# Optimization experiments

Hardware: AMD Instinct MI355X
Metric: run time of the kernel (lower is better)

The kernel has to match this reference:

```python
import jax, jax.numpy as jnp
import numpy as np

B, SQ, SK = 2, 2048, 2048
D = 1024            # in_features == num_heads * head_size
H, HS = 16, 64      # num_heads, head_size
SCALE = HS ** -0.5


def setup_inputs() -> dict:
    key = jax.random.key(0)
    ks = jax.random.split(key, 10)
    s = 0.02
    return {
        "inputs": jax.random.normal(ks[0], (B, SQ, D), jnp.float32),
        "context": jax.random.normal(ks[1], (B, SK, D), jnp.float32),
        "Wq": jax.random.normal(ks[2], (D, D), jnp.float32) * s,
        "bq": jnp.zeros((D,), jnp.float32),
        "Wk": jax.random.normal(ks[3], (D, D), jnp.float32) * s,
        "bk": jnp.zeros((D,), jnp.float32),
        "Wv": jax.random.normal(ks[4], (D, D), jnp.float32) * s,
        "bv": jnp.zeros((D,), jnp.float32),
        "Wo": jax.random.normal(ks[5], (D, D), jnp.float32) * s,
        "bo": jnp.zeros((D,), jnp.float32),
    }


def reference(inputs, context, Wq, bq, Wk, bk, Wv, bv, Wo, bo):
    # QKV projections (torch Linear: x @ W.T + b; here W stored as [in, out])
    q = inputs @ Wq + bq            # [B, SQ, D]
    k = context @ Wk + bk           # [B, SK, D]
    v = context @ Wv + bv           # [B, SK, D]
    q = q.reshape(B, SQ, H, HS)
    k = k.reshape(B, SK, H, HS)
    v = v.reshape(B, SK, H, HS)
    # scores: [B, H, SQ, SK] -- full score matrix materialized (as in source)
    score = jnp.einsum("bqhd,bkhd->bhqk", q, k) * SCALE
    weights = jax.nn.softmax(score, axis=-1)
    attn = jnp.einsum("bhqk,bkhd->bqhd", weights, v)  # [B, SQ, H, HS]
    out = attn.reshape(B, SQ, H * HS)
    return out @ Wo + bo
```

## Files before the change

kernel.cpp:

```cpp
#include <hip/hip_runtime.h>

#define BB 2
#define SQ 2048
#define SK 2048
#define DD 1024
#define HH 16
#define HS 64
#define SCALE 0.125f
#define LOG2E 1.4426950408889634f

typedef __bf16 bf16x8 __attribute__((ext_vector_type(8)));
typedef float f32x4 __attribute__((ext_vector_type(4)));
typedef unsigned int uint;

#if defined(__has_builtin)
#if __has_builtin(__builtin_amdgcn_exp2f)
#define FEXP2(x) __builtin_amdgcn_exp2f(x)
#endif
#endif
#ifndef FEXP2
extern "C" __device__ float __ocml_native_exp2_f32(float);
#define FEXP2(x) __ocml_native_exp2_f32(x)
#endif

__device__ __forceinline__ void gload_lds16(const __bf16* g, __bf16* l) {
    __builtin_amdgcn_global_load_lds((const __attribute__((address_space(1))) uint*)(g),
                                     (__attribute__((address_space(3))) uint*)(l), 16, 0, 0);
}

__global__ void cast2_f32_bf16(const float* __restrict__ in0, const float* __restrict__ in1,
                               __bf16* __restrict__ out0, __bf16* __restrict__ out1, int n8each) {
    int i = blockIdx.x * blockDim.x + threadIdx.x;
    const float* src;
    __bf16* dst;
    int j;
    if (i < n8each) { src = in0; dst = out0; j = i; }
    else            { src = in1; dst = out1; j = i - n8each; }
    const float4* p = ((const float4*)src) + (size_t)j * 2;
    float4 a = p[0], b = p[1];
    bf16x8 v = {(__bf16)a.x, (__bf16)a.y, (__bf16)a.z, (__bf16)a.w,
                (__bf16)b.x, (__bf16)b.y, (__bf16)b.z, (__bf16)b.w};
    ((bf16x8*)dst)[j] = v;
}

__global__ void wtrans(const float* __restrict__ W0, const float* __restrict__ W1,
                       const float* __restrict__ W2, const float* __restrict__ W3,
                       __bf16* __restrict__ Wt) {
    __shared__ __bf16 tile[32][33];
    const float* W = blockIdx.z == 0 ? W0 : blockIdx.z == 1 ? W1 : blockIdx.z == 2 ? W2 : W3;
    __bf16* out = Wt + (size_t)blockIdx.z * DD * DD;
    int tx = threadIdx.x, ty = threadIdx.y;
    int k0 = blockIdx.y * 32, n0 = blockIdx.x * 32;
#pragma unroll
    for (int j = 0; j < 4; ++j)
        tile[ty + j * 8][tx] = (__bf16)W[(size_t)(k0 + ty + j * 8) * DD + n0 + tx];
    __syncthreads();
#pragma unroll
    for (int j = 0; j < 4; ++j)
        out[(size_t)(n0 + ty + j * 8) * DD + k0 + tx] = tile[tx][ty + j * 8];
}

#define BM 128
#define BN2 64
#define BK 64
template <int MODE>
__device__ __forceinline__ void gemm_body(__bf16 (* __restrict__ As)[BK], __bf16 (* __restrict__ Bs)[BK],
                                          const __bf16* __restrict__ A, const __bf16* __restrict__ Bt,
                                          const float* __restrict__ bias, void* __restrict__ Cout,
                                          float scale) {
    int t = threadIdx.x;
    int w = t >> 6, l = t & 63;
    int lm = l & 15, lk = l >> 4;
    int wr = w >> 1, wc = w & 1;
    int br = blockIdx.y, bc = blockIdx.x;
    int srow = (l >> 3), scol = (l & 7) * 8;
    f32x4 acc[4][2] = {};
    for (int kt = 0; kt < 1024; kt += BK) {
        __syncthreads();
#pragma unroll
        for (int j = 0; j < 4; ++j) {
            int r0 = (w * 4 + j) * 8;
            gload_lds16(&A[(size_t)(br * BM + r0 + srow) * 1024 + kt + scol], &As[r0][0]);
        }
#pragma unroll
        for (int j = 0; j < 2; ++j) {
            int r0 = (w * 2 + j) * 8;
            gload_lds16(&Bt[(size_t)(bc * BN2 + r0 + srow) * 1024 + kt + scol], &Bs[r0][0]);
        }
        __syncthreads();
#pragma unroll
        for (int kk = 0; kk < BK; kk += 32) {
            bf16x8 af[4], bf[2];
#pragma unroll
            for (int m = 0; m < 4; ++m) af[m] = *(const bf16x8*)&As[wr * 64 + m * 16 + lm][kk + lk * 8];
#pragma unroll
            for (int n = 0; n < 2; ++n) bf[n] = *(const bf16x8*)&Bs[wc * 32 + n * 16 + lm][kk + lk * 8];
#pragma unroll
            for (int m = 0; m < 4; ++m)
#pragma unroll
                for (int n = 0; n < 2; ++n)
                    acc[m][n] = __builtin_amdgcn_mfma_f32_16x16x32_bf16(af[m], bf[n], acc[m][n], 0, 0, 0);
        }
    }
#pragma unroll
    for (int m = 0; m < 4; ++m)
#pragma unroll
        for (int n = 0; n < 2; ++n) {
            int col = bc * BN2 + wc * 32 + n * 16 + lm;
            float bv = bias[col];
            if constexpr (MODE == 2) {
                int row = br * BM + wr * 64 + m * 16 + lk * 4;
                int b_ = row >> 11, sk = row & 2047;
                int skb = sk & ~63, o = sk & 63;
                int p0 = (o & 32) | (((o >> 3) & 1) << 4) | (((o >> 2) & 1) << 3) | (((o >> 4) & 1) << 2);
                int h_ = col >> 6, d_ = col & 63;
                union { ushort4 u; __bf16 h[4]; } pk;
#pragma unroll
                for (int r = 0; r < 4; ++r) pk.h[r] = (__bf16)(acc[m][n][r] + bv);
                *(ushort4*)((__bf16*)Cout + ((size_t)((b_ * 16 + h_) * 64 + d_) * 2048 + skb + p0)) = pk.u;
            } else {
#pragma unroll
                for (int r = 0; r < 4; ++r) {
                    int row = br * BM + wr * 64 + m * 16 + lk * 4 + r;
                    ((__bf16*)Cout)[(size_t)row * 1024 + col] = (__bf16)((acc[m][n][r] + bv) * scale);
                }
            }
        }
}

__global__ __launch_bounds__(256) void gemm_qkv(const __bf16* __restrict__ Ain, const __bf16* __restrict__ Actx,
                                                const __bf16* __restrict__ Wt,
                                                const float* __restrict__ bq, const float* __restrict__ bk,
                                                const float* __restrict__ bv,
                                                __bf16* __restrict__ Qb, __bf16* __restrict__ Kb,
                                                __bf16* __restrict__ Vtb, float qscale) {
    __shared__ __bf16 As[BM][BK];
    __shared__ __bf16 Bs[BN2][BK];
    int z = blockIdx.z;
    const __bf16* A = (z == 0) ? Ain : Actx;
    const __bf16* B = Wt + (size_t)z * DD * DD;
    if (z == 0)      gemm_body<0>(As, Bs, A, B, bq, Qb, qscale);
    else if (z == 1) gemm_body<0>(As, Bs, A, B, bk, Kb, 1.f);
    else             gemm_body<2>(As, Bs, A, B, bv, Vtb, 1.f);
}

__global__ __launch_bounds__(256) void gemm_out64(const __bf16* __restrict__ A, const __bf16* __restrict__ Bt,
                                                  const float* __restrict__ bias, float* __restrict__ C) {
    __shared__ __bf16 As[64][64];
    __shared__ __bf16 Bs[128][64];
    int t = threadIdx.x;
    int w = t >> 6, l = t & 63;
    int lm = l & 15, lk = l >> 4;
    int br = blockIdx.y, bc = blockIdx.x;
    int srow = (l >> 3), scol = (l & 7) * 8;
    f32x4 acc[4][2] = {};
    for (int kt = 0; kt < 1024; kt += 64) {
        __syncthreads();
#pragma unroll
        for (int j = 0; j < 2; ++j) {
            int r0 = (j * 4 + w) * 8;
            gload_lds16(&A[(size_t)(br * 64 + r0 + srow) * 1024 + kt + scol], &As[r0][0]);
        }
#pragma unroll
        for (int j = 0; j < 4; ++j) {
            int r0 = (j * 4 + w) * 8;
            gload_lds16(&Bt[(size_t)(bc * 128 + r0 + srow) * 1024 + kt + scol], &Bs[r0][0]);
        }
        __syncthreads();
#pragma unroll
        for (int kk = 0; kk < 64; kk += 32) {
            bf16x8 af[4], bf[2];
#pragma unroll
            for (int m = 0; m < 4; ++m) af[m] = *(const bf16x8*)&As[m * 16 + lm][kk + lk * 8];
#pragma unroll
            for (int n = 0; n < 2; ++n) bf[n] = *(const bf16x8*)&Bs[w * 32 + n * 16 + lm][kk + lk * 8];
#pragma unroll
            for (int m = 0; m < 4; ++m)
#pragma unroll
                for (int n = 0; n < 2; ++n)
                    acc[m][n] = __builtin_amdgcn_mfma_f32_16x16x32_bf16(af[m], bf[n], acc[m][n], 0, 0, 0);
        }
    }
#pragma unroll
    for (int m = 0; m < 4; ++m)
#pragma unroll
        for (int n = 0; n < 2; ++n) {
            int col = bc * 128 + w * 32 + n * 16 + lm;
            float bv = bias[col];
#pragma unroll
            for (int r = 0; r < 4; ++r) {
                int row = br * 64 + m * 16 + lk * 4 + r;
                C[(size_t)row * 1024 + col] = acc[m][n][r] + bv;
            }
        }
}

__global__ __launch_bounds__(512) void flash_attn(const __bf16* __restrict__ Q,
                                                  const __bf16* __restrict__ Kb,
                                                  const __bf16* __restrict__ Vt,
                                                  __bf16* __restrict__ O) {
    __shared__ __bf16 Ks[2][64 * 64];
    __shared__ __bf16 Vs[2][64 * 64];
    int t = threadIdx.x, w = t >> 6, l = t & 63;
    int lm = l & 15, lk = l >> 4;
    int bh = blockIdx.y, b = bh >> 4, h = bh & 15;
    int q0 = blockIdx.x * 128;

    bf16x8 qf[2];
#pragma unroll
    for (int kk = 0; kk < 2; ++kk)
        qf[kk] = *(const bf16x8*)&Q[(size_t)(b * SQ + q0 + w * 16 + lm) * DD + h * HS + kk * 32 + lk * 8];

    int r0 = t >> 3, c8 = t & 7;
    int chs = c8 ^ (r0 & 7);
    __bf16* ksl0 = &Ks[0][r0 * 64 + chs * 8];
    __bf16* vsl0 = &Vs[0][r0 * 64 + chs * 8];

    const __bf16* kp0 = Kb + (size_t)b * SK * DD + h * HS + (size_t)r0 * DD + c8 * 8;
    const __bf16* vp0 = Vt + (size_t)bh * HS * SK + (size_t)r0 * SK + c8 * 8;

    int o0 = lm * 64 + ((lk ^ (lm & 7)) * 8);
    int o1 = lm * 64 + (((4 + lk) ^ (lm & 7)) * 8);

    float4 kr0, vr0;
#define FA_LOAD()                                                                \
    kr0 = *(const float4*)kp0; vr0 = *(const float4*)vp0;                        \
    kp0 += (size_t)64 * DD; vp0 += 64;
#define FA_WRITE(BUF)                                                            \
    *(float4*)(ksl0 + (BUF) * 4096) = kr0;                                       \
    *(float4*)(vsl0 + (BUF) * 4096) = vr0;

    FA_LOAD();
    FA_WRITE(0);
    __syncthreads();

    bf16x8 ones;
#pragma unroll
    for (int j = 0; j < 8; ++j) ones[j] = (__bf16)1.0f;

    f32x4 o[4] = {};
    f32x4 o_s = {};

    for (int it = 0; it < 32; ++it) {
        int buf = it & 1;
        if (it + 1 < 32) { FA_LOAD(); }

        const __bf16* KsB = &Ks[buf][0];
        const __bf16* VsB = &Vs[buf][0];

        f32x4 st[4] = {};
        __builtin_amdgcn_s_setprio(1);
#pragma unroll
        for (int kk = 0; kk < 2; ++kk) {
#pragma unroll
            for (int n = 0; n < 4; ++n) {
                bf16x8 kf = *(const bf16x8*)&KsB[(kk ? o1 : o0) + n * 1024];
                st[n] = __builtin_amdgcn_mfma_f32_16x16x32_bf16(kf, qf[kk], st[n], 0, 0, 0);
            }
        }
        __builtin_amdgcn_s_setprio(0);

#pragma unroll
        for (int kk = 0; kk < 2; ++kk) {
            bf16x8 pa;
#pragma unroll
            for (int j = 0; j < 8; ++j)
                pa[j] = (__bf16)FEXP2(st[2 * kk + (j >> 2)][j & 3]);
            __builtin_amdgcn_s_setprio(1);
            o_s = __builtin_amdgcn_mfma_f32_16x16x32_bf16(pa, ones, o_s, 0, 0, 0);
#pragma unroll
            for (int dn = 0; dn < 4; ++dn) {
                bf16x8 vf = *(const bf16x8*)&VsB[(kk ? o1 : o0) + dn * 1024];
                o[dn] = __builtin_amdgcn_mfma_f32_16x16x32_bf16(pa, vf, o[dn], 0, 0, 0);
            }
            __builtin_amdgcn_s_setprio(0);
        }

        if (it + 1 < 32) { FA_WRITE(buf ^ 1); }
        __syncthreads();
    }

    f32x4 inv;
#pragma unroll
    for (int r = 0; r < 4; ++r) inv[r] = 1.f / o_s[r];
#pragma unroll
    for (int dn = 0; dn < 4; ++dn)
#pragma unroll
        for (int r = 0; r < 4; ++r) {
            int row = q0 + w * 16 + lk * 4 + r;
            int col = h * HS + dn * 16 + lm;
            O[(size_t)(b * SQ + row) * DD + col] = (__bf16)(o[dn][r] * inv[r]);
        }
}

extern "C" void kernel_launch(void* const* d_in, const int* in_sizes, int n_in,
                              void* d_out, int out_size, void* d_ws, size_t ws_size,
                              hipStream_t stream) {
    const float* inputs  = (const float*)d_in[0];
    const float* context = (const float*)d_in[1];
    const float* Wq = (const float*)d_in[2];
    const float* bq = (const float*)d_in[3];
    const float* Wk = (const float*)d_in[4];
    const float* bk = (const float*)d_in[5];
    const float* Wv = (const float*)d_in[6];
    const float* bv = (const float*)d_in[7];
    const float* Wo = (const float*)d_in[8];
    const float* bo = (const float*)d_in[9];
    float* out = (float*)d_out;

    char* ws = (char*)d_ws;
    const size_t SEG = (size_t)4096 * 1024 * sizeof(__bf16);
    __bf16* inA  = (__bf16*)(ws + 0 * SEG);
    __bf16* ctxB = (__bf16*)(ws + 1 * SEG);
    __bf16* Wt   = (__bf16*)(ws + 2 * SEG);
    __bf16* Qb   = (__bf16*)(ws + 3 * SEG);
    __bf16* Kbuf = (__bf16*)(ws + 4 * SEG);
    __bf16* Vtb  = (__bf16*)(ws + 5 * SEG);
    __bf16* attb = ctxB;

    int n8 = 4096 * 1024 / 8;
    cast2_f32_bf16<<<2 * n8 / 256, 256, 0, stream>>>(inputs, context, inA, ctxB, n8);
    wtrans<<<dim3(32, 32, 4), dim3(32, 8), 0, stream>>>(Wq, Wk, Wv, Wo, Wt);

    gemm_qkv<<<dim3(16, 32, 3), 256, 0, stream>>>(inA, ctxB, Wt, bq, bk, bv,
                                                  Qb, Kbuf, Vtb, SCALE * LOG2E);

    flash_attn<<<dim3(16, 32), 512, 0, stream>>>(Qb, Kbuf, Vtb, attb);

    gemm_out64<<<dim3(8, 64), 256, 0, stream>>>(attb, Wt + (size_t)3 * DD * DD, bo, out);
}
```

Measured before the change: 127.9 us.

## Fuse fp32-to-bf16 activation cast into QKV GEMM and remap block order

```diff
diff --git a/kernel.cpp b/kernel.cpp
--- a/kernel.cpp
+++ b/kernel.cpp
@@ -28,21 +28,6 @@
                                      (__attribute__((address_space(3))) uint*)(l), 16, 0, 0);
 }
 
-__global__ void cast2_f32_bf16(const float* __restrict__ in0, const float* __restrict__ in1,
-                               __bf16* __restrict__ out0, __bf16* __restrict__ out1, int n8each) {
-    int i = blockIdx.x * blockDim.x + threadIdx.x;
-    const float* src;
-    __bf16* dst;
-    int j;
-    if (i < n8each) { src = in0; dst = out0; j = i; }
-    else            { src = in1; dst = out1; j = i - n8each; }
-    const float4* p = ((const float4*)src) + (size_t)j * 2;
-    float4 a = p[0], b = p[1];
-    bf16x8 v = {(__bf16)a.x, (__bf16)a.y, (__bf16)a.z, (__bf16)a.w,
-                (__bf16)b.x, (__bf16)b.y, (__bf16)b.z, (__bf16)b.w};
-    ((bf16x8*)dst)[j] = v;
-}
-
 __global__ void wtrans(const float* __restrict__ W0, const float* __restrict__ W1,
                        const float* __restrict__ W2, const float* __restrict__ W3,
                        __bf16* __restrict__ Wt) {
@@ -65,34 +50,61 @@
 #define BK 64
 template <int MODE>
 __device__ __forceinline__ void gemm_body(__bf16 (* __restrict__ As)[BK], __bf16 (* __restrict__ Bs)[BK],
-                                          const __bf16* __restrict__ A, const __bf16* __restrict__ Bt,
+                                          const float* __restrict__ Af, const __bf16* __restrict__ Bt,
                                           const float* __restrict__ bias, void* __restrict__ Cout,
                                           float scale) {
     int t = threadIdx.x;
     int w = t >> 6, l = t & 63;
     int lm = l & 15, lk = l >> 4;
     int wr = w >> 1, wc = w & 1;
-    int br = blockIdx.y, bc = blockIdx.x;
-    int srow = (l >> 3), scol = (l & 7) * 8;
+    int flat = blockIdx.x + 16 * blockIdx.y;
+    int nf = (flat & 7) * 64 + (flat >> 3);
+    int bc = nf & 15, br = nf >> 4;
+    int srow = l >> 3, sc8 = l & 7;
+
+    const float* ag = Af + (size_t)(br * BM + w * 32 + srow) * 1024 + sc8 * 8;
+    __bf16* aw = &As[w * 32 + srow][(sc8 ^ srow) * 8];
+
+    float4 xa0, xa1, xb0, xb1, xc0, xc1, xd0, xd1;
+#define GA_LOAD(KT)                                                                   \
+    xa0 = *(const float4*)(ag + (KT));          xa1 = *(const float4*)(ag + (KT) + 4);\
+    xb0 = *(const float4*)(ag + 8192 + (KT));   xb1 = *(const float4*)(ag + 8192 + (KT) + 4);\
+    xc0 = *(const float4*)(ag + 16384 + (KT));  xc1 = *(const float4*)(ag + 16384 + (KT) + 4);\
+    xd0 = *(const float4*)(ag + 24576 + (KT));  xd1 = *(const float4*)(ag + 24576 + (KT) + 4);
+#define GA_WRITE()                                                                    \
+    {                                                                                 \
+        bf16x8 va = {(__bf16)xa0.x, (__bf16)xa0.y, (__bf16)xa0.z, (__bf16)xa0.w,      \
+                     (__bf16)xa1.x, (__bf16)xa1.y, (__bf16)xa1.z, (__bf16)xa1.w};     \
+        bf16x8 vb = {(__bf16)xb0.x, (__bf16)xb0.y, (__bf16)xb0.z, (__bf16)xb0.w,      \
+                     (__bf16)xb1.x, (__bf16)xb1.y, (__bf16)xb1.z, (__bf16)xb1.w};     \
+        bf16x8 vc = {(__bf16)xc0.x, (__bf16)xc0.y, (__bf16)xc0.z, (__bf16)xc0.w,      \
+                     (__bf16)xc1.x, (__bf16)xc1.y, (__bf16)xc1.z, (__bf16)xc1.w};     \
+        bf16x8 vd = {(__bf16)xd0.x, (__bf16)xd0.y, (__bf16)xd0.z, (__bf16)xd0.w,      \
+                     (__bf16)xd1.x, (__bf16)xd1.y, (__bf16)xd1.z, (__bf16)xd1.w};     \
+        *(bf16x8*)(aw)        = va;                                                   \
+        *(bf16x8*)(aw + 512)  = vb;                                                   \
+        *(bf16x8*)(aw + 1024) = vc;                                                   \
+        *(bf16x8*)(aw + 1536) = vd;                                                   \
+    }
+
     f32x4 acc[4][2] = {};
+    GA_LOAD(0);
     for (int kt = 0; kt < 1024; kt += BK) {
         __syncthreads();
-#pragma unroll
-        for (int j = 0; j < 4; ++j) {
-            int r0 = (w * 4 + j) * 8;
-            gload_lds16(&A[(size_t)(br * BM + r0 + srow) * 1024 + kt + scol], &As[r0][0]);
-        }
+        GA_WRITE();
 #pragma unroll
         for (int j = 0; j < 2; ++j) {
             int r0 = (w * 2 + j) * 8;
-            gload_lds16(&Bt[(size_t)(bc * BN2 + r0 + srow) * 1024 + kt + scol], &Bs[r0][0]);
-        }
-        __syncthreads();
+            gload_lds16(&Bt[(size_t)(bc * BN2 + r0 + srow) * 1024 + kt + sc8 * 8], &Bs[r0][0]);
+        }
+        __syncthreads();
+        if (kt + BK < 1024) { GA_LOAD(kt + BK); }
 #pragma unroll
         for (int kk = 0; kk < BK; kk += 32) {
             bf16x8 af[4], bf[2];
 #pragma unroll
-            for (int m = 0; m < 4; ++m) af[m] = *(const bf16x8*)&As[wr * 64 + m * 16 + lm][kk + lk * 8];
+            for (int m = 0; m < 4; ++m)
+                af[m] = *(const bf16x8*)&As[wr * 64 + m * 16 + lm][((((kk >> 3) + lk)) ^ (lm & 7)) * 8];
 #pragma unroll
             for (int n = 0; n < 2; ++n) bf[n] = *(const bf16x8*)&Bs[wc * 32 + n * 16 + lm][kk + lk * 8];
 #pragma unroll
@@ -126,9 +138,11 @@
                 }
             }
         }
-}
-
-__global__ __launch_bounds__(256) void gemm_qkv(const __bf16* __restrict__ Ain, const __bf16* __restrict__ Actx,
+#undef GA_LOAD
+#undef GA_WRITE
+}
+
+__global__ __launch_bounds__(256) void gemm_qkv(const float* __restrict__ Ain, const float* __restrict__ Actx,
                                                 const __bf16* __restrict__ Wt,
                                                 const float* __restrict__ bq, const float* __restrict__ bk,
                                                 const float* __restrict__ bv,
@@ -137,7 +151,7 @@
     __shared__ __bf16 As[BM][BK];
     __shared__ __bf16 Bs[BN2][BK];
     int z = blockIdx.z;
-    const __bf16* A = (z == 0) ? Ain : Actx;
+    const float* A = (z == 0) ? Ain : Actx;
     const __bf16* B = Wt + (size_t)z * DD * DD;
     if (z == 0)      gemm_body<0>(As, Bs, A, B, bq, Qb, qscale);
     else if (z == 1) gemm_body<0>(As, Bs, A, B, bk, Kb, 1.f);
@@ -151,7 +165,9 @@
     int t = threadIdx.x;
     int w = t >> 6, l = t & 63;
     int lm = l & 15, lk = l >> 4;
-    int br = blockIdx.y, bc = blockIdx.x;
+    int flat = blockIdx.x + 8 * blockIdx.y;
+    int nf = (flat & 7) * 64 + (flat >> 3);
+    int bc = nf & 7, br = nf >> 3;
     int srow = (l >> 3), scol = (l & 7) * 8;
     f32x4 acc[4][2] = {};
     for (int kt = 0; kt < 1024; kt += 64) {
@@ -203,8 +219,10 @@
     __shared__ __bf16 Vs[2][64 * 64];
     int t = threadIdx.x, w = t >> 6, l = t & 63;
     int lm = l & 15, lk = l >> 4;
-    int bh = blockIdx.y, b = bh >> 4, h = bh & 15;
-    int q0 = blockIdx.x * 128;
+    int flat = blockIdx.x + 16 * blockIdx.y;
+    int nf = (flat & 7) * 64 + (flat >> 3);
+    int bh = nf >> 4, b = bh >> 4, h = bh & 15;
+    int q0 = (nf & 15) * 128;
 
     bf16x8 qf[2];
 #pragma unroll
@@ -310,19 +328,15 @@
 
     char* ws = (char*)d_ws;
     const size_t SEG = (size_t)4096 * 1024 * sizeof(__bf16);
-    __bf16* inA  = (__bf16*)(ws + 0 * SEG);
-    __bf16* ctxB = (__bf16*)(ws + 1 * SEG);
+    __bf16* attb = (__bf16*)(ws + 0 * SEG);
     __bf16* Wt   = (__bf16*)(ws + 2 * SEG);
     __bf16* Qb   = (__bf16*)(ws + 3 * SEG);
     __bf16* Kbuf = (__bf16*)(ws + 4 * SEG);
     __bf16* Vtb  = (__bf16*)(ws + 5 * SEG);
-    __bf16* attb = ctxB;
-
-    int n8 = 4096 * 1024 / 8;
-    cast2_f32_bf16<<<2 * n8 / 256, 256, 0, stream>>>(inputs, context, inA, ctxB, n8);
+
     wtrans<<<dim3(32, 32, 4), dim3(32, 8), 0, stream>>>(Wq, Wk, Wv, Wo, Wt);
 
-    gemm_qkv<<<dim3(16, 32, 3), 256, 0, stream>>>(inA, ctxB, Wt, bq, bk, bv,
+    gemm_qkv<<<dim3(16, 32, 3), 256, 0, stream>>>(inputs, context, Wt, bq, bk, bv,
                                                   Qb, Kbuf, Vtb, SCALE * LOG2E);
 
     flash_attn<<<dim3(16, 32), 512, 0, stream>>>(Qb, Kbuf, Vtb, attb);
```

Result: faster. 124.8 us (-2.5%).
